# Kernel tuning notes

Measured on AMD Instinct MI355X. Metric: run time of the kernel, lower is better.

The kernel has to match this reference:

```python
import jax, jax.numpy as jnp
import numpy as np

THRESH = 0.05
MAX_PER_IMAGE = 50
NMS_THRESH = 0.3
BBOX_STD = jnp.array([0.1, 0.1, 0.2, 0.2], dtype=jnp.float32)  # TRAIN.BBOX_NORMALIZE_STDS


def _decode_boxes(rois, deltas, im_info):
    """bbox_transform_inv + clip_boxes + rescale. rois [N,5], deltas [N,4C], im_info [3]=(h,w,scale).
    Returns [N,C,4] boxes in original-image coordinates."""
    boxes = rois[:, 1:5]
    w = boxes[:, 2] - boxes[:, 0] + 1.0
    h = boxes[:, 3] - boxes[:, 1] + 1.0
    cx = boxes[:, 0] + 0.5 * w
    cy = boxes[:, 1] + 0.5 * h
    d = deltas.reshape(deltas.shape[0], -1, 4) * BBOX_STD  # [N,C,4] (unnormalize deltas)
    dx, dy, dw, dh = d[..., 0], d[..., 1], d[..., 2], d[..., 3]
    pcx = dx * w[:, None] + cx[:, None]
    pcy = dy * h[:, None] + cy[:, None]
    pw = jnp.exp(dw) * w[:, None]
    ph = jnp.exp(dh) * h[:, None]
    x1 = jnp.clip(pcx - 0.5 * pw, 0.0, im_info[1] - 1.0)
    y1 = jnp.clip(pcy - 0.5 * ph, 0.0, im_info[0] - 1.0)
    x2 = jnp.clip(pcx + 0.5 * pw, 0.0, im_info[1] - 1.0)
    y2 = jnp.clip(pcy + 0.5 * ph, 0.0, im_info[0] - 1.0)
    return jnp.stack([x1, y1, x2, y2], axis=-1) / im_info[2]


def _nms(boxes, scores, valid):
    """Greedy NMS, fixed shapes. boxes [N,4], scores [N], valid bool [N].
    Returns (boxes_sorted [N,4], kept_scores [N] with -inf for dropped)."""
    n = boxes.shape[0]
    masked = jnp.where(valid, scores, -jnp.inf)
    order = jnp.argsort(-masked)
    b = boxes[order]
    s = masked[order]
    v = valid[order]
    x1, y1, x2, y2 = b[:, 0], b[:, 1], b[:, 2], b[:, 3]
    area = (x2 - x1 + 1.0) * (y2 - y1 + 1.0)
    ix1 = jnp.maximum(x1[:, None], x1[None, :])
    iy1 = jnp.maximum(y1[:, None], y1[None, :])
    ix2 = jnp.minimum(x2[:, None], x2[None, :])
    iy2 = jnp.minimum(y2[:, None], y2[None, :])
    iw = jnp.clip(ix2 - ix1 + 1.0, 0.0)
    ih = jnp.clip(iy2 - iy1 + 1.0, 0.0)
    inter = iw * ih
    iou = inter / (area[:, None] + area[None, :] - inter)  # [N,N]

    def step(keep, i):
        suppressed = jnp.any(keep & (iou[:, i] > NMS_THRESH))
        k = v[i] & jnp.logical_not(suppressed)
        return keep.at[i].set(k), k

    keep, _ = jax.lax.scan(step, jnp.zeros((n,), dtype=bool), jnp.arange(n))
    return b, jnp.where(keep, s, -jnp.inf)


def _per_image(rois, cls_prob, bbox_pred, im_info):
    """select_boxes for one image: decode, threshold, per-class NMS, global top max_per_image.
    Returns per-class best box [C-1,4] and best score [C-1] within the capped detection set."""
    boxes = _decode_boxes(rois, bbox_pred, im_info)  # [N,C,4]
    n, c = cls_prob.shape
    fg = c - 1

    def per_class(cb, cs):
        return _nms(cb, cs, cs > THRESH)

    fb, fs = jax.vmap(per_class, in_axes=(1, 1))(boxes[:, 1:, :], cls_prob[:, 1:])  # [C-1,N,4],[C-1,N]
    flat_s = fs.reshape(-1)
    flat_b = fb.reshape(-1, 4)
    topk_s, idx = jax.lax.top_k(flat_s, MAX_PER_IMAGE)  # global cap at max_per_image
    topk_b = flat_b[idx]
    topk_cls = idx // n  # fg class id of each kept detection
    # per-class best among kept detections (used by select_box)
    onehot = topk_cls[:, None] == jnp.arange(fg)[None, :]  # [max,fg]
    per_cls = jnp.where(onehot, topk_s[:, None], -jnp.inf)  # [max,fg]
    best_s = per_cls.max(axis=0)  # [fg]
    best_b = topk_b[per_cls.argmax(axis=0)]  # [fg,4]
    return best_b, best_s


def _select_boxes(rois, cls_prob, bbox_pred, im_infos):
    return jax.lax.map(lambda t: _per_image(*t), (rois, cls_prob, bbox_pred, im_infos))


def _forward(rois_A, cls_prob_A, bbox_pred_A, im_info_A, rois_B, cls_prob_B, bbox_pred_B, im_info_B):
    bA_b, bA_s = _select_boxes(rois_A, cls_prob_A, bbox_pred_A, im_info_A)  # [B,fg,4],[B,fg]
    bB_b, bB_s = _select_boxes(rois_B, cls_prob_B, bbox_pred_B, im_info_B)
    joint = bA_s * bB_s  # class must score well in BOTH images
    cls = jnp.argmax(joint, axis=1)  # [B]
    bidx = jnp.arange(joint.shape[0])
    box_A = jax.lax.stop_gradient(bA_b[bidx, cls])
    box_B = jax.lax.stop_gradient(bB_b[bidx, cls])
    return box_A, box_B


def setup_inputs() -> dict:
    key = jax.random.key(0)
    ks = jax.random.split(key, 6)
    B, N, C = 8, 2000, 21
    H, W = 600.0, 800.0

    def make_rois(k):
        k1, k2 = jax.random.split(k)
        xy = jax.random.uniform(k1, (B, N, 2)) * jnp.array([W - 1.0, H - 1.0])
        wh = jax.random.uniform(k2, (B, N, 2), minval=8.0, maxval=300.0)
        x2y2 = jnp.minimum(xy + wh, jnp.array([W - 1.0, H - 1.0]))
        bidx = jnp.zeros((B, N, 1))
        return jnp.concatenate([bidx, xy, x2y2], axis=-1).astype(jnp.float32)

    rois_A = make_rois(ks[0])
    rois_B = make_rois(ks[1])
    cls_prob_A = jax.nn.softmax(2.0 * jax.random.normal(ks[2], (B, N, C)), axis=-1).astype(jnp.float32)
    cls_prob_B = jax.nn.softmax(2.0 * jax.random.normal(ks[3], (B, N, C)), axis=-1).astype(jnp.float32)
    bbox_pred_A = (0.2 * jax.random.normal(ks[4], (B, N, 4 * C))).astype(jnp.float32)
    bbox_pred_B = (0.2 * jax.random.normal(ks[5], (B, N, 4 * C))).astype(jnp.float32)
    im_info = jnp.tile(jnp.array([[H, W, 1.0]], dtype=jnp.float32), (B, 1))
    return dict(rois_A=rois_A, cls_prob_A=cls_prob_A, bbox_pred_A=bbox_pred_A, im_info_A=im_info,
                rois_B=rois_B, cls_prob_B=cls_prob_B, bbox_pred_B=bbox_pred_B, im_info_B=im_info)


def reference(rois_A, cls_prob_A, bbox_pred_A, im_info_A, rois_B, cls_prob_B, bbox_pred_B, im_info_B):
    return _forward(rois_A, cls_prob_A, bbox_pred_A, im_info_A,
                    rois_B, cls_prob_B, bbox_pred_B, im_info_B)
```

## Files before the change

kernel.cpp:

```cpp
#include <hip/hip_runtime.h>
#include <stdint.h>
#include <math.h>

#define BNTH 256
#define CAP 1024
#define MAXK 50
#define THRESH_F 0.05f
#define NMS_T 0.3f
#define CMAX 24
#define SEGW_MAX 48

__device__ __forceinline__ void decode_box(
    const float* __restrict__ rois, const float* __restrict__ pred,
    float H, float W, float scale,
    int b, int n, int c, int N, int C, float out[4])
{
    const float* r = rois + ((size_t)b * N + n) * 5;
    float bx1 = r[1], by1 = r[2], bx2 = r[3], by2 = r[4];
    float w  = bx2 - bx1 + 1.0f;
    float h  = by2 - by1 + 1.0f;
    float cx = bx1 + 0.5f * w;
    float cy = by1 + 0.5f * h;
    const float* d = pred + ((size_t)b * N + n) * 4 * C + 4 * c;
    float dx = d[0] * 0.1f, dy = d[1] * 0.1f;
    float dw = d[2] * 0.2f, dh = d[3] * 0.2f;
    float pcx = dx * w + cx;
    float pcy = dy * h + cy;
    float pw  = expf(dw) * w;
    float ph  = expf(dh) * h;
    float X1 = fminf(fmaxf(pcx - 0.5f * pw, 0.0f), W - 1.0f);
    float Y1 = fminf(fmaxf(pcy - 0.5f * ph, 0.0f), H - 1.0f);
    float X2 = fminf(fmaxf(pcx + 0.5f * pw, 0.0f), W - 1.0f);
    float Y2 = fminf(fmaxf(pcy + 0.5f * ph, 0.0f), H - 1.0f);
    out[0] = X1 / scale;
    out[1] = Y1 / scale;
    out[2] = X2 / scale;
    out[3] = Y2 / scale;
}

__global__ __launch_bounds__(BNTH) void collect_kernel(
    const float* __restrict__ cls_A, const float* __restrict__ cls_B,
    int Bimg, int N, int C, int SEGW,
    int* __restrict__ scnt, unsigned long long* __restrict__ keys_ws)
{
    const int FG = C - 1;
    const int w = threadIdx.x >> 6;
    const int lane = threadIdx.x & 63;
    const int gw = blockIdx.x * 4 + w;
    const int nimg = 2 * Bimg;
    const int ib = gw / SEGW;
    const int seg = gw % SEGW;
    const bool live = (ib < nimg);

    __shared__ float tile[4][64 * CMAX];

    int n0 = 0, nrows = 0, b = 0, st = 0;
    const float* cls = cls_A;
    if (live) {
        st = ib >= Bimg;
        b = ib - st * Bimg;
        cls = st ? cls_B : cls_A;
        n0 = seg * 64;
        nrows = N - n0; nrows = nrows < 0 ? 0 : (nrows > 64 ? 64 : nrows);
    }

    float* tl = tile[w];
    const size_t gbase = ((size_t)b * N + n0) * C;
    const int tot = nrows * C;
    for (int e = lane; e < tot; e += 64) tl[e] = cls[gbase + e];
    __syncthreads();

    if (live) {
        for (int cc = 1; cc < C; ++cc) {
            const float sc = (lane < nrows) ? tl[lane * C + cc] : 0.0f;
            const bool val = sc > THRESH_F;
            const uint64_t bal = __ballot(val);
            const size_t task_seg = (size_t)(ib * SEGW + seg) * FG + (cc - 1);
            if (val) {
                const int slot = __popcll(bal & ((1ull << lane) - 1ull));
                keys_ws[task_seg * 64 + slot] =
                    ((uint64_t)__float_as_uint(sc) << 32) |
                    (uint32_t)(~(uint32_t)(n0 + lane));
            }
            if (lane == 0) scnt[task_seg] = __popcll(bal);
        }
    }
}

template<int SN>
__device__ __forceinline__ void bitonic_desc(double* kd, int lane)
{
    constexpr int NS = SN / 64;
    #pragma unroll
    for (int k = 2; k <= SN; k <<= 1) {
        #pragma unroll
        for (int j = k >> 1; j >= 1; j >>= 1) {
            if (j >= 64) {
                const int js = j >> 6;
                #pragma unroll
                for (int s = 0; s < NS; ++s) {
                    if ((s & js) == 0) {
                        const int sp = s | js;
                        const bool d = (((s << 6) & k) == 0);
                        const double a = kd[s], bb = kd[sp];
                        kd[s]  = d ? fmax(a, bb) : fmin(a, bb);
                        kd[sp] = d ? fmin(a, bb) : fmax(a, bb);
                    }
                }
            } else {
                #pragma unroll
                for (int s = 0; s < NS; ++s) {
                    const double o = __shfl_xor(kd[s], j);
                    const bool lower = (lane & j) == 0;
                    const bool d = ((((s << 6) | lane) & k) == 0);
                    const bool takeMax = (d == lower);
                    const double mx = fmax(kd[s], o);
                    const double mn = fmin(kd[s], o);
                    kd[s] = takeMax ? mx : mn;
                }
            }
        }
    }
}

__global__ __launch_bounds__(BNTH, 1) void nms_kernel(
    const float* __restrict__ rois_A, const float* __restrict__ pred_A,
    const float* __restrict__ info_A,
    const float* __restrict__ rois_B, const float* __restrict__ pred_B,
    const float* __restrict__ info_B,
    int Bimg, int N, int C, int SEGW,
    const int* __restrict__ scnt, const unsigned long long* __restrict__ keys_ws,
    float* __restrict__ kept_scores, int* __restrict__ kcounts,
    float* __restrict__ cls_box, int* __restrict__ sync_counter)
{
    const int FG = C - 1;
    const int bx = blockIdx.x;
    const int st  = bx / (Bimg * FG);
    const int rem = bx % (Bimg * FG);
    const int b = rem / FG;
    const int j = rem % FG;
    const int c = j + 1;
    const int tid = threadIdx.x;
    const int lane = tid & 63;
    const int ib = st * Bimg + b;

    if (bx == 0 && tid == 0) *sync_counter = 0;

    const float* rois = st ? rois_B : rois_A;
    const float* pred = st ? pred_B : pred_A;
    const float* info = st ? info_B : info_A;

    __shared__ uint64_t keysL[CAP];
    __shared__ float4 boxL[CAP];
    __shared__ float  sarL[CAP];
    __shared__ float4 keptL[MAXK];
    __shared__ int offL[SEGW_MAX + 1];

    if (tid < 64) {
        int v = 0;
        if (lane < SEGW) v = scnt[(size_t)(ib * SEGW + lane) * FG + j];
        #pragma unroll
        for (int d = 1; d < 64; d <<= 1) {
            const int o = __shfl_up(v, d);
            if (lane >= d) v += o;
        }
        if (lane < SEGW) offL[lane + 1] = v;
        if (lane == 0) offL[0] = 0;
    }
    __syncthreads();
    const int Mfull = offL[SEGW];
    const int M = Mfull < CAP ? Mfull : CAP;

    for (int i = tid; i < CAP; i += BNTH) {
        uint64_t k = 0ull;
        if (i < M) {
            int lo = 0, hi = SEGW;
            while (hi - lo > 1) {
                const int mid = (lo + hi) >> 1;
                if (offL[mid] <= i) lo = mid; else hi = mid;
            }
            k = keys_ws[((size_t)(ib * SEGW + lo) * FG + j) * 64 + (i - offL[lo])];
        }
        keysL[i] = k;
    }
    __syncthreads();

    if (tid < 64) {
        if (M > 1) {
            if (M <= 512) {
                double kd[8];
                #pragma unroll
                for (int s = 0; s < 8; ++s)
                    kd[s] = __longlong_as_double((long long)keysL[s * 64 + lane]);
                bitonic_desc<512>(kd, lane);
                #pragma unroll
                for (int s = 0; s < 8; ++s)
                    keysL[s * 64 + lane] = (uint64_t)__double_as_longlong(kd[s]);
            } else {
                double kd[16];
                #pragma unroll
                for (int s = 0; s < 16; ++s)
                    kd[s] = __longlong_as_double((long long)keysL[s * 64 + lane]);
                bitonic_desc<1024>(kd, lane);
                #pragma unroll
                for (int s = 0; s < 16; ++s)
                    keysL[s * 64 + lane] = (uint64_t)__double_as_longlong(kd[s]);
            }
        }
    }
    __syncthreads();

    const float H = info[b * 3 + 0];
    const float W = info[b * 3 + 1];
    const float scale = info[b * 3 + 2];
    for (int i = tid; i < M; i += BNTH) {
        const uint64_t u = keysL[i];
        const int n = (int)(~(uint32_t)u);
        float o[4];
        decode_box(rois, pred, H, W, scale, b, n, c, N, C, o);
        boxL[i] = make_float4(o[0], o[1], o[2], o[3]);
        sarL[i] = (o[2] - o[0] + 1.0f) * (o[3] - o[1] + 1.0f);
    }
    __syncthreads();

    if (tid < 64) {
        float* ksc = kept_scores + (size_t)bx * MAXK;
        int kcount = 0;
        float4 cls_best = make_float4(0.f, 0.f, 0.f, 0.f);

        for (int s = 0; s * 64 < M && kcount < MAXK; ++s) {
            const int ii = s * 64 + lane;
            const bool valid = (ii < M);
            float cx1 = 0.f, cy1 = 0.f, cx2 = 0.f, cy2 = 0.f, car = 1.0f, csc = 0.f;
            if (valid) {
                const float4 cb4 = boxL[ii];
                cx1 = cb4.x; cy1 = cb4.y; cx2 = cb4.z; cy2 = cb4.w;
                car = sarL[ii];
                csc = __uint_as_float((uint32_t)(keysL[ii] >> 32));
            }
            bool sup = !valid;
            for (int q = 0; q < kcount; ++q) {
                const float4 kb = keptL[q];
                const float kar = (kb.z - kb.x + 1.0f) * (kb.w - kb.y + 1.0f);
                const float ix1 = fmaxf(kb.x, cx1), iy1 = fmaxf(kb.y, cy1);
                const float ix2 = fminf(kb.z, cx2), iy2 = fminf(kb.w, cy2);
                const float iw = fmaxf(ix2 - ix1 + 1.0f, 0.0f);
                const float ih = fmaxf(iy2 - iy1 + 1.0f, 0.0f);
                const float inter = iw * ih;
                sup = sup || (inter / (kar + car - inter) > NMS_T);
            }
            uint64_t alive = ~__ballot(sup);
            while (alive != 0ull && kcount < MAXK) {
                const int l = __builtin_ctzll(alive);
                const float kx1 = __shfl(cx1, l), ky1 = __shfl(cy1, l);
                const float kx2 = __shfl(cx2, l), ky2 = __shfl(cy2, l);
                const float kar = (kx2 - kx1 + 1.0f) * (ky2 - ky1 + 1.0f);
                if (lane == l) {
                    keptL[kcount] = make_float4(cx1, cy1, cx2, cy2);
                    ksc[kcount] = csc;
                }
                if (kcount == 0) cls_best = make_float4(kx1, ky1, kx2, ky2);
                const float ix1 = fmaxf(kx1, cx1), iy1 = fmaxf(ky1, cy1);
                const float ix2 = fminf(kx2, cx2), iy2 = fminf(ky2, cy2);
                const float iw = fmaxf(ix2 - ix1 + 1.0f, 0.0f);
                const float ih = fmaxf(iy2 - iy1 + 1.0f, 0.0f);
                const float inter = iw * ih;
                const bool s2 = (inter / (kar + car - inter) > NMS_T);
                alive &= ~__ballot(s2);
                alive &= ~(1ull << l);
                kcount++;
            }
        }

        if (lane == 0) {
            kcounts[bx] = kcount;
            float* cbp = cls_box + (size_t)bx * 4;
            cbp[0] = cls_best.x; cbp[1] = cls_best.y;
            cbp[2] = cls_best.z; cbp[3] = cls_best.w;
        }
    }
}

__global__ __launch_bounds__(64) void select_combine(
    const float* __restrict__ kept_scores, const int* __restrict__ kcounts,
    const float* __restrict__ cls_box,
    const float* __restrict__ rois_A, const float* __restrict__ pred_A,
    const float* __restrict__ info_A,
    const float* __restrict__ rois_B, const float* __restrict__ pred_B,
    const float* __restrict__ info_B,
    int Bimg, int N, int C,
    float* best_s, float* best_b, int* sync_counter, float* __restrict__ out)
{
    const int FG = C - 1;
    const int bx = blockIdx.x;
    const int st = bx / Bimg;
    const int b  = bx % Bimg;
    const int tid = threadIdx.x;

    __shared__ float sk[20][MAXK];
    __shared__ int   skc[20];
    __shared__ float stopv[20];
    __shared__ int   cnt20[20];
    __shared__ int   inflag[20];
    __shared__ float gbox[4];
    __shared__ int   amlast;

    const size_t base = (size_t)bx * FG;
    for (int i = tid; i < FG * MAXK; i += 64)
        sk[i / MAXK][i % MAXK] = kept_scores[base * MAXK + i];
    if (tid < FG) {
        skc[tid] = kcounts[base + tid];
        cnt20[tid] = 0;
    }
    __syncthreads();
    if (tid < FG)
        stopv[tid] = (skc[tid] > 0) ? sk[tid][0] : -INFINITY;
    __syncthreads();

    for (int p = tid; p < FG * FG; p += 64) {
        const int cc = p / FG;
        const int c2 = p % FG;
        const float sc = stopv[cc];
        const int k2 = skc[c2];
        int cnt = 0;
        if (skc[cc] > 0) {
            #pragma unroll 5
            for (int k = 0; k < k2; ++k) {
                const float v = sk[c2][k];
                cnt += ((v > sc) || (v == sc && c2 < cc)) ? 1 : 0;
            }
        }
        if (cnt) atomicAdd(&cnt20[cc], cnt);
    }
    __syncthreads();
    if (tid < FG)
        inflag[tid] = (skc[tid] > 0 && cnt20[tid] < MAXK) ? 1 : 0;
    __syncthreads();

    if (tid == 0) {
        int g = -1;
        float bs = -INFINITY;
        for (int c2 = 0; c2 < FG; ++c2)
            if (skc[c2] > 0 && stopv[c2] > bs) { bs = stopv[c2]; g = c2; }
        if (g >= 0) {
            const float* cbp = cls_box + (base + g) * 4;
            gbox[0] = cbp[0]; gbox[1] = cbp[1]; gbox[2] = cbp[2]; gbox[3] = cbp[3];
        } else {
            const float* rois = st ? rois_B : rois_A;
            const float* pred = st ? pred_B : pred_A;
            const float* info = st ? info_B : info_A;
            decode_box(rois, pred, info[b * 3], info[b * 3 + 1], info[b * 3 + 2],
                       b, 0, 1, N, C, gbox);
        }
    }
    __syncthreads();

    if (tid < FG) {
        const int in = inflag[tid];
        best_s[base + tid] = in ? stopv[tid] : -INFINITY;
        float* ob = best_b + (base + tid) * 4;
        if (in) {
            const float* cbp = cls_box + (base + tid) * 4;
            ob[0] = cbp[0]; ob[1] = cbp[1]; ob[2] = cbp[2]; ob[3] = cbp[3];
        } else {
            ob[0] = gbox[0]; ob[1] = gbox[1]; ob[2] = gbox[2]; ob[3] = gbox[3];
        }
    }

    __threadfence();
    if (tid == 0) amlast = (atomicAdd(sync_counter, 1) == 2 * Bimg - 1);
    __syncthreads();
    if (amlast) {
        __threadfence();
        if (tid < Bimg) {
            const int i = tid;
            const float* sA = best_s + (size_t)i * FG;
            const float* sB = best_s + (size_t)(Bimg + i) * FG;
            float bj = 0.0f;
            int cls = 0;
            for (int cc = 0; cc < FG; ++cc) {
                const float v = sA[cc] * sB[cc];
                if (cc == 0 || v > bj) { bj = v; cls = cc; }
            }
            const float* bA = best_b + ((size_t)i * FG + cls) * 4;
            const float* bB = best_b + ((size_t)(Bimg + i) * FG + cls) * 4;
            for (int k = 0; k < 4; ++k) {
                out[i * 4 + k]            = bA[k];
                out[Bimg * 4 + i * 4 + k] = bB[k];
            }
        }
    }
}

extern "C" void kernel_launch(void* const* d_in, const int* in_sizes, int n_in,
                              void* d_out, int out_size, void* d_ws, size_t ws_size,
                              hipStream_t stream) {
    const float* rois_A = (const float*)d_in[0];
    const float* cls_A  = (const float*)d_in[1];
    const float* pred_A = (const float*)d_in[2];
    const float* info_A = (const float*)d_in[3];
    const float* rois_B = (const float*)d_in[4];
    const float* cls_B  = (const float*)d_in[5];
    const float* pred_B = (const float*)d_in[6];
    const float* info_B = (const float*)d_in[7];
    float* out = (float*)d_out;

    const int Bimg = in_sizes[3] / 3;
    const int N    = in_sizes[0] / (Bimg * 5);
    const int C    = in_sizes[1] / (Bimg * N);
    const int FG   = C - 1;
    const int NSB  = 2 * Bimg * FG;
    const int SEGW = (N + 63) / 64;

    char* ws = (char*)d_ws;
    int* sync_counter = (int*)ws;
    size_t off = 256;
    int* scnt = (int*)(ws + off);
    off += (size_t)2 * Bimg * SEGW * FG * sizeof(int);
    off = (off + 255) & ~(size_t)255;
    unsigned long long* keys_ws = (unsigned long long*)(ws + off);
    off += (size_t)2 * Bimg * SEGW * FG * 64 * sizeof(unsigned long long);
    float* kept_scores = (float*)(ws + off);
    off += (size_t)NSB * MAXK * sizeof(float);
    int* kcounts = (int*)(ws + off);
    off += (size_t)NSB * sizeof(int);
    float* cls_box = (float*)(ws + off);
    off += (size_t)NSB * 4 * sizeof(float);
    float* best_s = (float*)(ws + off);
    off += (size_t)NSB * sizeof(float);
    float* best_b = (float*)(ws + off);

    const int nwaves = 2 * Bimg * SEGW;
    collect_kernel<<<(nwaves + 3) / 4, BNTH, 0, stream>>>(
        cls_A, cls_B, Bimg, N, C, SEGW, scnt, keys_ws);

    nms_kernel<<<NSB, BNTH, 0, stream>>>(
        rois_A, pred_A, info_A, rois_B, pred_B, info_B,
        Bimg, N, C, SEGW, scnt, keys_ws, kept_scores, kcounts, cls_box,
        sync_counter);

    select_combine<<<2 * Bimg, 64, 0, stream>>>(
        kept_scores, kcounts, cls_box,
        rois_A, pred_A, info_A, rois_B, pred_B, info_B,
        Bimg, N, C, best_s, best_b, sync_counter, out);
}
```

Baseline: 61.59 us.

## Fuse score collection into NMS kernel using shared-memory segment keys

Removes the separate collect kernel and its global workspace of per-segment keys and counts. Each NMS block now reads its own class column of cls_prob directly, ballot-compacts the above-threshold scores per 64-row segment into shared memory, and builds the sorted key list from there. This drops one kernel launch and a global write/read round trip. In exchange each block performs strided column reads of cls_prob (stride C floats) and uses more shared memory per block.

```diff
diff --git a/kernel.cpp b/kernel.cpp
--- a/kernel.cpp
+++ b/kernel.cpp
@@ -7,7 +7,6 @@
 #define MAXK 50
 #define THRESH_F 0.05f
 #define NMS_T 0.3f
-#define CMAX 24
 #define SEGW_MAX 48
 
 __device__ __forceinline__ void decode_box(
@@ -38,55 +37,6 @@
     out[3] = Y2 / scale;
 }
 
-__global__ __launch_bounds__(BNTH) void collect_kernel(
-    const float* __restrict__ cls_A, const float* __restrict__ cls_B,
-    int Bimg, int N, int C, int SEGW,
-    int* __restrict__ scnt, unsigned long long* __restrict__ keys_ws)
-{
-    const int FG = C - 1;
-    const int w = threadIdx.x >> 6;
-    const int lane = threadIdx.x & 63;
-    const int gw = blockIdx.x * 4 + w;
-    const int nimg = 2 * Bimg;
-    const int ib = gw / SEGW;
-    const int seg = gw % SEGW;
-    const bool live = (ib < nimg);
-
-    __shared__ float tile[4][64 * CMAX];
-
-    int n0 = 0, nrows = 0, b = 0, st = 0;
-    const float* cls = cls_A;
-    if (live) {
-        st = ib >= Bimg;
-        b = ib - st * Bimg;
-        cls = st ? cls_B : cls_A;
-        n0 = seg * 64;
-        nrows = N - n0; nrows = nrows < 0 ? 0 : (nrows > 64 ? 64 : nrows);
-    }
-
-    float* tl = tile[w];
-    const size_t gbase = ((size_t)b * N + n0) * C;
-    const int tot = nrows * C;
-    for (int e = lane; e < tot; e += 64) tl[e] = cls[gbase + e];
-    __syncthreads();
-
-    if (live) {
-        for (int cc = 1; cc < C; ++cc) {
-            const float sc = (lane < nrows) ? tl[lane * C + cc] : 0.0f;
-            const bool val = sc > THRESH_F;
-            const uint64_t bal = __ballot(val);
-            const size_t task_seg = (size_t)(ib * SEGW + seg) * FG + (cc - 1);
-            if (val) {
-                const int slot = __popcll(bal & ((1ull << lane) - 1ull));
-                keys_ws[task_seg * 64 + slot] =
-                    ((uint64_t)__float_as_uint(sc) << 32) |
-                    (uint32_t)(~(uint32_t)(n0 + lane));
-            }
-            if (lane == 0) scnt[task_seg] = __popcll(bal);
-        }
-    }
-}
-
 template<int SN>
 __device__ __forceinline__ void bitonic_desc(double* kd, int lane)
 {
@@ -124,12 +74,11 @@
 }
 
 __global__ __launch_bounds__(BNTH, 1) void nms_kernel(
-    const float* __restrict__ rois_A, const float* __restrict__ pred_A,
-    const float* __restrict__ info_A,
-    const float* __restrict__ rois_B, const float* __restrict__ pred_B,
-    const float* __restrict__ info_B,
-    int Bimg, int N, int C, int SEGW,
-    const int* __restrict__ scnt, const unsigned long long* __restrict__ keys_ws,
+    const float* __restrict__ rois_A, const float* __restrict__ cls_A,
+    const float* __restrict__ pred_A, const float* __restrict__ info_A,
+    const float* __restrict__ rois_B, const float* __restrict__ cls_B,
+    const float* __restrict__ pred_B, const float* __restrict__ info_B,
+    int Bimg, int N, int C,
     float* __restrict__ kept_scores, int* __restrict__ kcounts,
     float* __restrict__ cls_box, int* __restrict__ sync_counter)
 {
@@ -141,24 +90,47 @@
     const int j = rem % FG;
     const int c = j + 1;
     const int tid = threadIdx.x;
+    const int w = tid >> 6;
     const int lane = tid & 63;
-    const int ib = st * Bimg + b;
+    const int SEGW = (N + 63) >> 6;
 
     if (bx == 0 && tid == 0) *sync_counter = 0;
 
     const float* rois = st ? rois_B : rois_A;
+    const float* cls  = st ? cls_B  : cls_A;
     const float* pred = st ? pred_B : pred_A;
     const float* info = st ? info_B : info_A;
 
+    __shared__ uint64_t segKeys[SEGW_MAX][64];
+    __shared__ int segCnt[SEGW_MAX];
+    __shared__ int offL[SEGW_MAX + 1];
     __shared__ uint64_t keysL[CAP];
     __shared__ float4 boxL[CAP];
     __shared__ float  sarL[CAP];
     __shared__ float4 keptL[MAXK];
-    __shared__ int offL[SEGW_MAX + 1];
+
+    const int ROUNDS = (SEGW + 3) >> 2;
+    for (int r = 0; r < ROUNDS; ++r) {
+        const int seg = w + 4 * r;
+        if (seg < SEGW) {
+            const int n = seg * 64 + lane;
+            float sc = 0.0f;
+            if (n < N) sc = cls[((size_t)b * N + n) * C + c];
+            const bool val = sc > THRESH_F;
+            const uint64_t bal = __ballot(val);
+            if (val) {
+                const int slot = __popcll(bal & ((1ull << lane) - 1ull));
+                segKeys[seg][slot] =
+                    ((uint64_t)__float_as_uint(sc) << 32) |
+                    (uint32_t)(~(uint32_t)n);
+            }
+            if (lane == 0) segCnt[seg] = __popcll(bal);
+        }
+    }
+    __syncthreads();
 
     if (tid < 64) {
-        int v = 0;
-        if (lane < SEGW) v = scnt[(size_t)(ib * SEGW + lane) * FG + j];
+        int v = (lane < SEGW) ? segCnt[lane] : 0;
         #pragma unroll
         for (int d = 1; d < 64; d <<= 1) {
             const int o = __shfl_up(v, d);
@@ -179,7 +151,7 @@
                 const int mid = (lo + hi) >> 1;
                 if (offL[mid] <= i) lo = mid; else hi = mid;
             }
-            k = keys_ws[((size_t)(ib * SEGW + lo) * FG + j) * 64 + (i - offL[lo])];
+            k = segKeys[lo][i - offL[lo]];
         }
         keysL[i] = k;
     }
@@ -410,16 +382,10 @@
     const int C    = in_sizes[1] / (Bimg * N);
     const int FG   = C - 1;
     const int NSB  = 2 * Bimg * FG;
-    const int SEGW = (N + 63) / 64;
 
     char* ws = (char*)d_ws;
     int* sync_counter = (int*)ws;
     size_t off = 256;
-    int* scnt = (int*)(ws + off);
-    off += (size_t)2 * Bimg * SEGW * FG * sizeof(int);
-    off = (off + 255) & ~(size_t)255;
-    unsigned long long* keys_ws = (unsigned long long*)(ws + off);
-    off += (size_t)2 * Bimg * SEGW * FG * 64 * sizeof(unsigned long long);
     float* kept_scores = (float*)(ws + off);
     off += (size_t)NSB * MAXK * sizeof(float);
     int* kcounts = (int*)(ws + off);
@@ -430,14 +396,10 @@
     off += (size_t)NSB * sizeof(float);
     float* best_b = (float*)(ws + off);
 
-    const int nwaves = 2 * Bimg * SEGW;
-    collect_kernel<<<(nwaves + 3) / 4, BNTH, 0, stream>>>(
-        cls_A, cls_B, Bimg, N, C, SEGW, scnt, keys_ws);
-
     nms_kernel<<<NSB, BNTH, 0, stream>>>(
-        rois_A, pred_A, info_A, rois_B, pred_B, info_B,
-        Bimg, N, C, SEGW, scnt, keys_ws, kept_scores, kcounts, cls_box,
-        sync_counter);
+        rois_A, cls_A, pred_A, info_A,
+        rois_B, cls_B, pred_B, info_B,
+        Bimg, N, C, kept_scores, kcounts, cls_box, sync_counter);
 
     select_combine<<<2 * Bimg, 64, 0, stream>>>(
         kept_scores, kcounts, cls_box,
```

After: 60.48 us. Within noise of the previous version (-1.8%).
